# Kernel tuning notes

Measured on AMD Instinct MI355X. Metric: run time of the kernel, lower is better.

## Reference

```python
import jax, jax.numpy as jnp
import numpy as np

N_CHR = 23
N_EMB = 512
E_DIM = 128
B = 4
L = 2048


def setup_inputs() -> dict:
    key = jax.random.key(0)
    k1, k2, k3 = jax.random.split(key, 3)
    chromosome = jax.random.randint(k1, (B, N_CHR, L), 0, N_CHR)
    position = jax.random.uniform(k2, (B, N_CHR, L), dtype=jnp.float32)
    embeddings = jax.random.normal(k3, (N_CHR, N_EMB, E_DIM), dtype=jnp.float32)
    centers = jnp.tile(jnp.linspace(0.0, 1.0, N_EMB, dtype=jnp.float32)[None, :], (N_CHR, 1))  # [23,512]
    log_variances = jnp.full((N_CHR, N_EMB), -5.0, dtype=jnp.float32)
    return {
        "chromosome": chromosome,
        "position": position,
        "embeddings": embeddings,
        "centers": centers,
        "log_variances": log_variances,
    }


def reference(chromosome, position, embeddings, centers, log_variances):
    # position: [B, C=23, L]; centers/log_variances: [C, K=512]; embeddings: [C, K, E]
    variances = jnp.exp(log_variances)                       # [C, K]
    d = position[..., None] - centers[None, :, None, :]      # [B, C, L, K]
    rbf = jnp.exp(-(d * d) / (2.0 * variances[None, :, None, :]))
    weights = jax.nn.softmax(rbf, axis=-1)                   # softmax over codebook (matches torch)
    out = jnp.einsum("bclk,cke->bcle", weights, embeddings)  # [B, C, L, E]
    bsz = position.shape[0]
    return out.reshape(bsz, -1, embeddings.shape[-1])        # [B, C*L, E]
```

## Files before the change

### kernel.cpp

```cpp
#include <hip/hip_runtime.h>
#include <hip/hip_bf16.h>

#define N_CHR 23
#define N_EMB 512
#define E_DIM 128
#define B_SZ  4
#define L_SEQ 2048
#define LOG2E 1.4426950408889634f

typedef __attribute__((ext_vector_type(8))) short short8;
typedef __attribute__((ext_vector_type(4))) float floatx4;

#if __has_builtin(__builtin_amdgcn_exp2f)
#define EXP2(x) __builtin_amdgcn_exp2f(x)
#else
#define EXP2(x) __expf((x) * 0.6931471805599453f)
#endif

__device__ __forceinline__ float bf2f(unsigned short u) {
    return __uint_as_float(((unsigned)u) << 16);
}
__device__ __forceinline__ unsigned short f2bf(float f) {
    unsigned u = __float_as_uint(f);
    unsigned r = u + 0x7FFFu + ((u >> 16) & 1u);
    return (unsigned short)(r >> 16);
}

__global__ __launch_bounds__(256) void emb_pack_kernel(
    const float* __restrict__ emb, uint4* __restrict__ embw)
{
    const int idx  = blockIdx.x * 256 + threadIdx.x;
    const int lane = idx & 63;
    const int nt   = (idx >> 6) & 7;
    const int ch   = (idx >> 9) & 15;
    const int c    = idx >> 13;
    if (c >= N_CHR) return;
    const int quad = lane >> 4;
    const int n    = nt * 16 + (lane & 15);
    const float* src = emb + (size_t)(c * N_EMB + ch * 32 + quad * 8) * E_DIM + n;
    unsigned v[8];
#pragma unroll
    for (int j = 0; j < 8; ++j) v[j] = (unsigned)f2bf(src[j * E_DIM]);
    uint4 w;
    w.x = v[0] | (v[1] << 16);
    w.y = v[2] | (v[3] << 16);
    w.z = v[4] | (v[5] << 16);
    w.w = v[6] | (v[7] << 16);
    embw[idx] = w;
}

__global__ __launch_bounds__(256, 4) void rbf_emb_kernel(
    const float* __restrict__ pos,
    const uint4* __restrict__ embw,
    const float* __restrict__ ctr,
    const float* __restrict__ lvar,
    float* __restrict__ out)
{
    __shared__ float2 cs_s[N_EMB];
    __shared__ uint4 Bs[2][512];
    __shared__ float inv_s[64];

    const int tid  = threadIdx.x;
    const int lane = tid & 63;
    const int wave = tid >> 6;
    const int quad = lane >> 4;
    const int m    = lane & 15;

    const int bc   = blockIdx.x >> 5;
    const int mt   = blockIdx.x & 31;
    const int c    = bc % N_CHR;
    const int row0 = mt * 64;

    for (int k = tid; k < N_EMB; k += 256) {
        cs_s[k] = make_float2(ctr[c * N_EMB + k],
                              -0.5f * LOG2E * __expf(-lvar[c * N_EMB + k]));
    }

    const int   myrow = row0 + wave * 16 + m;
    const float posf  = pos[bc * L_SEQ + myrow];

    floatx4 acc[8];
#pragma unroll
    for (int i = 0; i < 8; ++i) acc[i] = (floatx4){0.f, 0.f, 0.f, 0.f};
    float denom = 0.f;

    __syncthreads();

    const uint4*  gbase = embw + (size_t)c * (16 * 8 * 64);
    const float2* csq   = cs_s + quad * 8;

    for (int ch = 0; ch < 16; ++ch) {
        const int kc = ch * 32;
        uint4* bw = Bs[ch & 1];

        {
            const uint4* g = gbase + ch * 512 + wave * 128 + lane;
            __builtin_amdgcn_global_load_lds(
                (const __attribute__((address_space(1))) void*)(g),
                (__attribute__((address_space(3))) void*)(bw + wave * 128), 16, 0, 0);
            __builtin_amdgcn_global_load_lds(
                (const __attribute__((address_space(1))) void*)(g + 64),
                (__attribute__((address_space(3))) void*)(bw + wave * 128 + 64), 16, 0, 0);
        }

        unsigned pk[4];
#pragma unroll
        for (int jj = 0; jj < 4; ++jj) {
            const float2 cs0 = csq[kc + 2 * jj];
            const float2 cs1 = csq[kc + 2 * jj + 1];
            const float d0 = posf - cs0.x;
            const float d1 = posf - cs1.x;
            const float p0 = EXP2(EXP2(d0 * d0 * cs0.y) * LOG2E);
            const float p1 = EXP2(EXP2(d1 * d1 * cs1.y) * LOG2E);
            const unsigned u0 = __float_as_uint(p0);
            const unsigned u1 = __float_as_uint(p1);
            const unsigned r0 = (u0 + 0x7FFFu + ((u0 >> 16) & 1u)) >> 16;
            const unsigned r1 = (u1 + 0x7FFFu + ((u1 >> 16) & 1u)) & 0xFFFF0000u;
            pk[jj] = r0 | r1;
            denom += __uint_as_float(r0 << 16) + __uint_as_float(r1);
        }
        const int4 pkv = make_int4((int)pk[0], (int)pk[1], (int)pk[2], (int)pk[3]);
        const short8 afrag = __builtin_bit_cast(short8, pkv);

        __syncthreads();

        const uint4* br = bw;
#pragma unroll
        for (int nt = 0; nt < 8; ++nt) {
            short8 bfrag = *(const short8*)&br[(nt << 6) + lane];
            acc[nt] = __builtin_amdgcn_mfma_f32_16x16x32_bf16(afrag, bfrag, acc[nt], 0, 0, 0);
        }
    }

    denom += __shfl_xor(denom, 16);
    denom += __shfl_xor(denom, 32);
    if (lane < 16) inv_s[wave * 16 + m] = 1.0f / denom;
    __syncthreads();

    float* outp = out + (size_t)(bc * L_SEQ + row0 + wave * 16) * E_DIM;
#pragma unroll
    for (int reg = 0; reg < 4; ++reg) {
        const int   r   = quad * 4 + reg;
        const float inv = inv_s[wave * 16 + r];
        float* o = outp + r * E_DIM + m;
#pragma unroll
        for (int nt = 0; nt < 8; ++nt) {
            o[nt * 16] = acc[nt][reg] * inv;
        }
    }
}

__global__ __launch_bounds__(256, 4) void rbf_emb_kernel_slow(
    const float* __restrict__ pos, const float* __restrict__ emb,
    const float* __restrict__ ctr, const float* __restrict__ lvar,
    float* __restrict__ out)
{
    __shared__ float centers_s[N_EMB];
    __shared__ float scale_s[N_EMB];
    __shared__ uint4 Bs[2][512];
    __shared__ float inv_s[64];

    const int tid  = threadIdx.x;
    const int lane = tid & 63;
    const int wave = tid >> 6;
    const int quad = lane >> 4;
    const int m    = lane & 15;
    const int bc   = blockIdx.x >> 5;
    const int mt   = blockIdx.x & 31;
    const int c    = bc % N_CHR;
    const int row0 = mt * 64;

    for (int k = tid; k < N_EMB; k += 256) {
        centers_s[k] = ctr[c * N_EMB + k];
        scale_s[k]   = -0.5f * __expf(-lvar[c * N_EMB + k]);
    }
    const float posf = pos[bc * L_SEQ + row0 + wave * 16 + m];
    floatx4 acc[8];
#pragma unroll
    for (int i = 0; i < 8; ++i) acc[i] = (floatx4){0.f, 0.f, 0.f, 0.f};
    float denom = 0.f;
    __syncthreads();

    const int n_st = tid & 127;
    const int qd0  = tid >> 7;
    const float* embc = emb + (size_t)c * (N_EMB * E_DIM);

    for (int ch = 0; ch < 16; ++ch) {
        const int kc = ch * 32;
        uint4* bw = Bs[ch & 1];
#pragma unroll
        for (int qq = 0; qq < 2; ++qq) {
            const int qd = qd0 + qq * 2;
            const float* src = embc + (kc + qd * 8) * E_DIM + n_st;
            unsigned v[8];
#pragma unroll
            for (int j = 0; j < 8; ++j) v[j] = (unsigned)f2bf(src[j * E_DIM]);
            uint4 w;
            w.x = v[0] | (v[1] << 16);
            w.y = v[2] | (v[3] << 16);
            w.z = v[4] | (v[5] << 16);
            w.w = v[6] | (v[7] << 16);
            bw[((n_st >> 4) << 6) + (qd << 4) + (n_st & 15)] = w;
        }
        short8 afrag;
#pragma unroll
        for (int j = 0; j < 8; ++j) {
            const int   k   = kc + quad * 8 + j;
            const float d   = posf - centers_s[k];
            const float rbf = __expf(d * d * scale_s[k]);
            const float p   = __expf(rbf);
            const unsigned short pb = f2bf(p);
            afrag[j] = (short)pb;
            denom += bf2f(pb);
        }
        __syncthreads();
        const uint4* br = bw;
#pragma unroll
        for (int nt = 0; nt < 8; ++nt) {
            short8 bfrag = *(const short8*)&br[(nt << 6) + lane];
            acc[nt] = __builtin_amdgcn_mfma_f32_16x16x32_bf16(afrag, bfrag, acc[nt], 0, 0, 0);
        }
    }
    denom += __shfl_xor(denom, 16);
    denom += __shfl_xor(denom, 32);
    if (lane < 16) inv_s[wave * 16 + m] = 1.0f / denom;
    __syncthreads();
    float* outp = out + (size_t)(bc * L_SEQ + row0 + wave * 16) * E_DIM;
#pragma unroll
    for (int reg = 0; reg < 4; ++reg) {
        const int   r   = quad * 4 + reg;
        const float inv = inv_s[wave * 16 + r];
        float* o = outp + r * E_DIM + m;
#pragma unroll
        for (int nt = 0; nt < 8; ++nt) o[nt * 16] = acc[nt][reg] * inv;
    }
}

extern "C" void kernel_launch(void* const* d_in, const int* in_sizes, int n_in,
                              void* d_out, int out_size, void* d_ws, size_t ws_size,
                              hipStream_t stream) {
    const float* pos  = (const float*)d_in[1];
    const float* emb  = (const float*)d_in[2];
    const float* ctr  = (const float*)d_in[3];
    const float* lvar = (const float*)d_in[4];
    float* out = (float*)d_out;

    const int    blocks   = (B_SZ * N_CHR) * (L_SEQ / 64);
    const size_t ws_needed = (size_t)N_CHR * 16 * 8 * 64 * 16;

    if (ws_size >= ws_needed) {
        uint4* embw = (uint4*)d_ws;
        emb_pack_kernel<<<(N_CHR * 16 * 8 * 64) / 256, 256, 0, stream>>>(emb, embw);
        rbf_emb_kernel<<<blocks, 256, 0, stream>>>(pos, embw, ctr, lvar, out);
    } else {
        rbf_emb_kernel_slow<<<blocks, 256, 0, stream>>>(pos, emb, ctr, lvar, out);
    }
}
```

Before: 145.9 us.

## Prefetch embedding chunks ahead and compute softmax denominator via MFMA

Restructures the main loop so the next embedding chunk's async global-to-LDS load is issued one iteration ahead, and the next A fragment is computed after the current MFMAs, overlapping exp work with matrix ops. The softmax denominator is now computed by an extra MFMA against a ones vector instead of scalar adds and shuffles, which removes the shared inv_s buffer and a barrier. The exp argument folds the LOG2E multiply into an additive constant, uses packed float2 math and the hardware bf16 pack, and raises the occupancy hint to 7 blocks. The risks are register pressure from the higher occupancy target and small rounding differences from the new exponent formulation.

Result: no change. 145.9 us (+0.0%).

```diff
diff --git a/kernel.cpp b/kernel.cpp
--- a/kernel.cpp
+++ b/kernel.cpp
@@ -7,14 +7,22 @@
 #define B_SZ  4
 #define L_SEQ 2048
 #define LOG2E 1.4426950408889634f
+#define LOG2_LOG2E 0.5287663729448977f
 
 typedef __attribute__((ext_vector_type(8))) short short8;
 typedef __attribute__((ext_vector_type(4))) float floatx4;
+typedef __attribute__((ext_vector_type(2))) float f32x2;
 
 #if __has_builtin(__builtin_amdgcn_exp2f)
 #define EXP2(x) __builtin_amdgcn_exp2f(x)
 #else
 #define EXP2(x) __expf((x) * 0.6931471805599453f)
+#endif
+
+#if __has_builtin(__builtin_amdgcn_rcpf)
+#define RCP(x) __builtin_amdgcn_rcpf(x)
+#else
+#define RCP(x) (1.0f / (x))
 #endif
 
 __device__ __forceinline__ float bf2f(unsigned short u) {
@@ -49,7 +57,7 @@
     embw[idx] = w;
 }
 
-__global__ __launch_bounds__(256, 4) void rbf_emb_kernel(
+__global__ __launch_bounds__(256, 7) void rbf_emb_kernel(
     const float* __restrict__ pos,
     const uint4* __restrict__ embw,
     const float* __restrict__ ctr,
@@ -58,7 +66,6 @@
 {
     __shared__ float2 cs_s[N_EMB];
     __shared__ uint4 Bs[2][512];
-    __shared__ float inv_s[64];
 
     const int tid  = threadIdx.x;
     const int lane = tid & 63;
@@ -71,30 +78,64 @@
     const int c    = bc % N_CHR;
     const int row0 = mt * 64;
 
+    const uint4* gbase = embw + (size_t)c * (16 * 8 * 64);
+
+    {
+        const uint4* g = gbase + wave * 128 + lane;
+        __builtin_amdgcn_global_load_lds(
+            (const __attribute__((address_space(1))) void*)(g),
+            (__attribute__((address_space(3))) void*)(&Bs[0][wave * 128]), 16, 0, 0);
+        __builtin_amdgcn_global_load_lds(
+            (const __attribute__((address_space(1))) void*)(g + 64),
+            (__attribute__((address_space(3))) void*)(&Bs[0][wave * 128 + 64]), 16, 0, 0);
+    }
+
     for (int k = tid; k < N_EMB; k += 256) {
         cs_s[k] = make_float2(ctr[c * N_EMB + k],
                               -0.5f * LOG2E * __expf(-lvar[c * N_EMB + k]));
     }
 
-    const int   myrow = row0 + wave * 16 + m;
-    const float posf  = pos[bc * L_SEQ + myrow];
+    const float posf = pos[bc * L_SEQ + row0 + wave * 16 + m];
 
     floatx4 acc[8];
 #pragma unroll
     for (int i = 0; i < 8; ++i) acc[i] = (floatx4){0.f, 0.f, 0.f, 0.f};
-    float denom = 0.f;
+    floatx4 accd = (floatx4){0.f, 0.f, 0.f, 0.f};
+
+    short8 bones;
+#pragma unroll
+    for (int j = 0; j < 8; ++j) bones[j] = (short)0x3F80;
+
+    auto computeA = [&](int ch) -> short8 {
+        const float4* cs4 = ((const float4*)cs_s) + ch * 16 + quad * 4;
+        unsigned pk[4];
+#pragma unroll
+        for (int jj = 0; jj < 4; ++jj) {
+            const float4 q = cs4[jj];
+            f32x2 cc = {q.x, q.z};
+            f32x2 ss = {q.y, q.w};
+            f32x2 d  = (f32x2){posf, posf} - cc;
+            f32x2 t  = d * d;
+            t = t * ss + (f32x2){LOG2_LOG2E, LOG2_LOG2E};
+            const float p0 = EXP2(EXP2(t.x));
+            const float p1 = EXP2(EXP2(t.y));
+            union { __hip_bfloat162 h; unsigned u; } cv;
+            cv.h = __float22bfloat162_rn(make_float2(p0, p1));
+            pk[jj] = cv.u;
+        }
+        const int4 v = make_int4((int)pk[0], (int)pk[1], (int)pk[2], (int)pk[3]);
+        return __builtin_bit_cast(short8, v);
+    };
 
     __syncthreads();
-
-    const uint4*  gbase = embw + (size_t)c * (16 * 8 * 64);
-    const float2* csq   = cs_s + quad * 8;
+    short8 aNext = computeA(0);
 
     for (int ch = 0; ch < 16; ++ch) {
-        const int kc = ch * 32;
-        uint4* bw = Bs[ch & 1];
-
-        {
-            const uint4* g = gbase + ch * 512 + wave * 128 + lane;
+        __syncthreads();
+
+        if (ch < 15) {
+            const uint4* g = gbase + (ch + 1) * 512 + wave * 128 + lane;
+            uint4* bw = Bs[(ch + 1) & 1];
             __builtin_amdgcn_global_load_lds(
                 (const __attribute__((address_space(1))) void*)(g),
                 (__attribute__((address_space(3))) void*)(bw + wave * 128), 16, 0, 0);
@@ -103,46 +144,24 @@
                 (__attribute__((address_space(3))) void*)(bw + wave * 128 + 64), 16, 0, 0);
         }
 
-        unsigned pk[4];
-#pragma unroll
-        for (int jj = 0; jj < 4; ++jj) {
-            const float2 cs0 = csq[kc + 2 * jj];
-            const float2 cs1 = csq[kc + 2 * jj + 1];
-            const float d0 = posf - cs0.x;
-            const float d1 = posf - cs1.x;
-            const float p0 = EXP2(EXP2(d0 * d0 * cs0.y) * LOG2E);
-            const float p1 = EXP2(EXP2(d1 * d1 * cs1.y) * LOG2E);
-            const unsigned u0 = __float_as_uint(p0);
-            const unsigned u1 = __float_as_uint(p1);
-            const unsigned r0 = (u0 + 0x7FFFu + ((u0 >> 16) & 1u)) >> 16;
-            const unsigned r1 = (u1 + 0x7FFFu + ((u1 >> 16) & 1u)) & 0xFFFF0000u;
-            pk[jj] = r0 | r1;
-            denom += __uint_as_float(r0 << 16) + __uint_as_float(r1);
-        }
-        const int4 pkv = make_int4((int)pk[0], (int)pk[1], (int)pk[2], (int)pk[3]);
-        const short8 afrag = __builtin_bit_cast(short8, pkv);
-
-        __syncthreads();
-
-        const uint4* br = bw;
+        const short8 a = aNext;
+        const uint4* br = Bs[ch & 1];
+
+        accd = __builtin_amdgcn_mfma_f32_16x16x32_bf16(a, bones, accd, 0, 0, 0);
 #pragma unroll
         for (int nt = 0; nt < 8; ++nt) {
             short8 bfrag = *(const short8*)&br[(nt << 6) + lane];
-            acc[nt] = __builtin_amdgcn_mfma_f32_16x16x32_bf16(afrag, bfrag, acc[nt], 0, 0, 0);
-        }
-    }
-
-    denom += __shfl_xor(denom, 16);
-    denom += __shfl_xor(denom, 32);
-    if (lane < 16) inv_s[wave * 16 + m] = 1.0f / denom;
-    __syncthreads();
+            acc[nt] = __builtin_amdgcn_mfma_f32_16x16x32_bf16(a, bfrag, acc[nt], 0, 0, 0);
+        }
+
+        if (ch < 15) aNext = computeA(ch + 1);
+    }
 
     float* outp = out + (size_t)(bc * L_SEQ + row0 + wave * 16) * E_DIM;
 #pragma unroll
     for (int reg = 0; reg < 4; ++reg) {
-        const int   r   = quad * 4 + reg;
-        const float inv = inv_s[wave * 16 + r];
-        float* o = outp + r * E_DIM + m;
+        const float inv = RCP(accd[reg]);
+        float* o = outp + (quad * 4 + reg) * E_DIM + m;
 #pragma unroll
         for (int nt = 0; nt < 8; ++nt) {
             o[nt * 16] = acc[nt][reg] * inv;
@@ -245,7 +264,7 @@
     const float* lvar = (const float*)d_in[4];
     float* out = (float*)d_out;
 
-    const int    blocks   = (B_SZ * N_CHR) * (L_SEQ / 64);
+    const int    blocks    = (B_SZ * N_CHR) * (L_SEQ / 64);
     const size_t ws_needed = (size_t)N_CHR * 16 * 8 * 64 * 16;
 
     if (ws_size >= ws_needed) {
```
